# Performance work log

Measured on AMD Instinct MI355X. Metric: run time of the kernel, lower is better.

## Reference

```python
import jax, jax.numpy as jnp
import numpy as np

N_NODES = 50000
N_EDGES = 800000
IN_CH = 128
HEADS = 4
OUT_CH = 32


def setup_inputs() -> dict:
    key = jax.random.key(0)
    k1, k2, k3, k4 = jax.random.split(key, 4)
    x = jax.random.normal(k1, (N_NODES, IN_CH), dtype=jnp.float32)
    edge_index = jax.random.randint(k2, (2, N_EDGES), 0, N_NODES, dtype=jnp.int64)
    # nn.Linear weight [out, in] with xavier-uniform init
    limW = float(np.sqrt(6.0 / (IN_CH + HEADS * OUT_CH)))
    W = jax.random.uniform(k3, (HEADS * OUT_CH, IN_CH), minval=-limW, maxval=limW, dtype=jnp.float32)
    lima = float(np.sqrt(6.0 / (HEADS + 2 * OUT_CH)))
    att = jax.random.uniform(k4, (HEADS, 2 * OUT_CH), minval=-lima, maxval=lima, dtype=jnp.float32)
    bias = jnp.zeros((HEADS * OUT_CH,), dtype=jnp.float32)
    return {"x": x, "edge_index": edge_index, "W": W, "att": att, "bias": bias}


def reference(x, edge_index, W, att, bias):
    n = x.shape[0]
    heads, two_c = att.shape
    out_ch = two_c // 2
    loop = jnp.arange(n, dtype=edge_index.dtype)
    src = jnp.concatenate([edge_index[0], loop])  # [E+n]
    dst = jnp.concatenate([edge_index[1], loop])  # [E+n]
    h = (x @ W.T).reshape(n, heads, out_ch)       # [n, H, C]
    h_src = h[src]                                # [E+n, H, C]
    h_dst = h[dst]                                # [E+n, H, C]
    # e = sum over channels of att applied to [h_src || h_dst]
    e = (jnp.einsum('ehc,hc->eh', h_src, att[:, :out_ch])
         + jnp.einsum('ehc,hc->eh', h_dst, att[:, out_ch:]))  # [E+n, H]
    e = jax.nn.leaky_relu(e, negative_slope=0.2)
    # segment softmax over incoming edges per dst node
    e_max = jax.ops.segment_max(e, dst, num_segments=n)        # [n, H]
    alpha = jnp.exp(e - e_max[dst])                            # [E+n, H]
    a_sum = jax.ops.segment_sum(alpha, dst, num_segments=n)    # [n, H]
    alpha = alpha / jnp.maximum(a_sum[dst], 1e-10)
    weighted = h_src * alpha[..., None]                        # [E+n, H, C]
    out = jax.ops.segment_sum(weighted, dst, num_segments=n)   # [n, H, C]
    out = out.reshape(n, heads * out_ch)                       # concat=True
    return out + bias
```

## Files before the change

kernel.cpp:

```cpp
#include <hip/hip_runtime.h>
#include <hip/hip_bf16.h>
#include <math.h>

#define N_NODES 50000
#define N_EDGES 800000
#define IN_CH   128
#define HEADS   4
#define OUT_CH  32
#define HC      128
#define WROWS   136

#define CB_SHIFT 7
#define CB_NODES 128
#define N_CB     391
#define NBK      128
#define EPB      (N_EDGES / NBK)
#define PCAP     44
#define ND_CAP   48
#define CB_CAP   2560

#define NG_TOT   782
#define NG_A     586
#define NG_B     (NG_TOT - NG_A)

typedef __attribute__((ext_vector_type(8))) short short8;
typedef __attribute__((ext_vector_type(4))) float floatx4;

__device__ __forceinline__ short f2bf(float f) {
    __hip_bfloat16 h = __float2bfloat16(f);
    return *reinterpret_cast<short*>(&h);
}

__global__ __launch_bounds__(256) void kP_prep(
    const float* __restrict__ W, const float* __restrict__ att,
    unsigned short* __restrict__ Wb) {

    const int tid = threadIdx.x;

    {
        int row  = tid >> 1;
        int half = tid & 1;
        const float4* Wr = (const float4*)(W + row * IN_CH + half * 64);
        unsigned short* dp = Wb + row * WROWS + half * 64;
#pragma unroll
        for (int i = 0; i < 16; ++i) {
            float4 v = Wr[i];
            ushort4 p;
            p.x = (unsigned short)f2bf(v.x);
            p.y = (unsigned short)f2bf(v.y);
            p.z = (unsigned short)f2bf(v.z);
            p.w = (unsigned short)f2bf(v.w);
            *(ushort4*)(dp + i * 4) = p;
        }
    }

#pragma unroll
    for (int k = 0; k < 4; ++k) {
        int idx  = tid + k * 256;
        int j    = idx >> 7;
        int i    = idx & 127;
        int head = j & 3;
        int aoff = (j & 4) ? 32 : 0;
        float s = 0.f;
#pragma unroll
        for (int c = 0; c < 32; ++c)
            s = fmaf(W[(head * 32 + c) * IN_CH + i], att[head * 64 + aoff + c], s);
        Wb[(128 + j) * WROWS + i] = (unsigned short)f2bf(s);
    }

    for (int z = tid; z < 8 * WROWS; z += 256) Wb[136 * WROWS + z] = 0;
}

__device__ __forceinline__ void gemm_role(
    short* __restrict__ Wlds, int node_base,
    const float* __restrict__ x, const unsigned short* __restrict__ Wb,
    __hip_bfloat16* __restrict__ hbuf,
    float* __restrict__ asrc, float* __restrict__ adst) {

    const int tid  = threadIdx.x;
    const int wave = tid >> 6;
    const int lane = tid & 63;
    const int col  = lane & 15;
    const int q    = lane >> 4;

#pragma unroll
    for (int i = 0; i < 10; ++i) {
        int off = ((i << 2) + wave) * 64 + lane;
        ((float4*)Wlds)[off] = ((const float4*)Wb)[off];
    }
    __syncthreads();

    const int node0 = node_base + wave * 16;
    const int m  = node0 + col;
    const int mc = min(m, N_NODES - 1);

    floatx4 acc[9];
#pragma unroll
    for (int t = 0; t < 9; ++t) acc[t] = (floatx4){0.f, 0.f, 0.f, 0.f};

#pragma unroll
    for (int ks = 0; ks < 4; ++ks) {
        const float4* xp = (const float4*)(x + (size_t)mc * IN_CH + ks * 32 + q * 8);
        float4 v0 = xp[0];
        float4 v1 = xp[1];
        short8 af;
        af[0] = f2bf(v0.x); af[1] = f2bf(v0.y); af[2] = f2bf(v0.z); af[3] = f2bf(v0.w);
        af[4] = f2bf(v1.x); af[5] = f2bf(v1.y); af[6] = f2bf(v1.z); af[7] = f2bf(v1.w);
#pragma unroll
        for (int t = 0; t < 9; ++t) {
            const short8 bf = *(const short8*)(Wlds + (t * 16 + col) * WROWS + ks * 32 + q * 8);
            acc[t] = __builtin_amdgcn_mfma_f32_16x16x32_bf16(af, bf, acc[t], 0, 0, 0);
        }
    }

#pragma unroll
    for (int r = 0; r < 4; ++r) {
        const int node = node0 + q * 4 + r;
        if (node >= N_NODES) continue;
#pragma unroll
        for (int t = 0; t < 8; ++t)
            hbuf[(size_t)node * HC + t * 16 + col] = __float2bfloat16(acc[t][r]);
        float v8 = acc[8][r];
        if (col < 4)      asrc[node * HEADS + col] = v8;
        else if (col < 8) adst[node * HEADS + col - 4] = v8;
    }
}

__global__ __launch_bounds__(256) void kA_fused(
    const int* __restrict__ src, const int* __restrict__ dst,
    unsigned* __restrict__ priv, int* __restrict__ cnt2,
    const float* __restrict__ x, const unsigned short* __restrict__ Wb,
    __hip_bfloat16* __restrict__ hbuf,
    float* __restrict__ asrc, float* __restrict__ adst) {

    __shared__ float4 smem4[2560];
    const int tid = threadIdx.x;

    if (blockIdx.x < NBK) {
        int* lcnt = (int*)smem4;
        const int blk = blockIdx.x;
        for (int i = tid; i < N_CB; i += 256) lcnt[i] = 0;
        __syncthreads();

        const int e0 = blk * EPB;
        for (int e = e0 + tid; e < e0 + EPB; e += 256) {
            int s = src[e];
            int d = dst[e];
            int cb = d >> CB_SHIFT;
            int pos = atomicAdd(&lcnt[cb], 1);
            if (pos < PCAP)
                priv[((size_t)cb * NBK + blk) * PCAP + pos] =
                    ((unsigned)(d & (CB_NODES - 1)) << 16) | (unsigned)s;
        }
        __syncthreads();
        for (int i = tid; i < N_CB; i += 256)
            cnt2[blk * N_CB + i] = min(lcnt[i], PCAP);
        return;
    }

    gemm_role((short*)smem4, (blockIdx.x - NBK) * 64, x, Wb, hbuf, asrc, adst);
}

__global__ __launch_bounds__(256) void kB_fused(
    const int* __restrict__ cnt2, const unsigned* __restrict__ priv,
    unsigned short* __restrict__ csr16, unsigned* __restrict__ meta,
    const float* __restrict__ x, const unsigned short* __restrict__ Wb,
    __hip_bfloat16* __restrict__ hbuf,
    float* __restrict__ asrc, float* __restrict__ adst) {

    __shared__ float4 smem4[2560];
    const int tid = threadIdx.x;

    if (blockIdx.x >= N_CB) {
        gemm_role((short*)smem4, (NG_A + (int)blockIdx.x - N_CB) * 64,
                  x, Wb, hbuf, asrc, adst);
        return;
    }

    char* smem = (char*)smem4;
    unsigned short* list = (unsigned short*)smem;
    int* lcnt  = (int*)(smem + 12800);
    int* ccnt  = (int*)(smem + 13312);
    int* lpre  = (int*)(smem + 13824);
    int* lcnt2 = (int*)(smem + 14336);

    const int b = blockIdx.x;
    const int node0 = b << CB_SHIFT;
    const int nInB  = min(CB_NODES, N_NODES - node0);

    if (tid < CB_NODES) lcnt[tid] = 0;
    if (tid < NBK) lcnt2[tid] = cnt2[tid * N_CB + b];
    __syncthreads();

    const unsigned* p = priv + (size_t)b * NBK * PCAP;
    for (int idx = tid; idx < NBK * PCAP; idx += 256) {
        int blk = (idx * 5958) >> 18;
        int j   = idx - blk * PCAP;
        if (j < lcnt2[blk]) {
            unsigned ent = p[idx];
            int dl   = ent >> 16;
            int slot = atomicAdd(&lcnt[dl], 1);
            if (slot < ND_CAP) list[dl * ND_CAP + slot] = (unsigned short)(ent & 0xFFFFu);
        }
    }
    __syncthreads();

    if (tid < CB_NODES) { ccnt[tid] = min(lcnt[tid], ND_CAP); lpre[tid] = ccnt[tid]; }
    __syncthreads();
    for (int d = 1; d < CB_NODES; d <<= 1) {
        int v = (tid >= d && tid < CB_NODES) ? lpre[tid - d] : 0;
        __syncthreads();
        if (tid < CB_NODES) lpre[tid] += v;
        __syncthreads();
    }

    if (tid < nInB) {
        int cnt  = ccnt[tid];
        int excl = lpre[tid] - cnt;
        meta[node0 + tid] = (unsigned)(b * CB_CAP + excl) | ((unsigned)cnt << 24);
    }

    const int total = lpre[CB_NODES - 1];
    __syncthreads();
    for (int idx = tid; idx < total; idx += 256) {
        int n = 0;
#pragma unroll
        for (int s = 64; s; s >>= 1)
            if (idx >= lpre[n + s - 1]) n += s;
        int j = idx - (lpre[n] - ccnt[n]);
        csr16[b * CB_CAP + idx] = list[n * ND_CAP + j];
    }
}

__device__ __forceinline__ float edge_w(float t) {
    t = fmaxf(t, 0.2f * t);
    return __expf(t);
}

__global__ __launch_bounds__(256) void kb6_agg(
    const unsigned* __restrict__ meta, const unsigned short* __restrict__ csr16,
    const unsigned* __restrict__ hb, const float* __restrict__ asrc,
    const float* __restrict__ adst, const float* __restrict__ bias,
    float* __restrict__ out) {

    const int node = __builtin_amdgcn_readfirstlane(blockIdx.x * 4 + (threadIdx.x >> 6));
    if (node >= N_NODES) return;
    const int lane = threadIdx.x & 63;
    const int h    = lane >> 4;

    const unsigned mt = meta[node];
    const int cnt = (int)(mt >> 24);
    const unsigned short* p = csr16 + (mt & 0xFFFFFFu);

    const float ad = adst[node * HEADS + h];

    unsigned us = hb[node * 64 + lane];
    float wS = edge_w(asrc[node * HEADS + h] + ad);
    float ds = wS;
    float ax = wS * __uint_as_float(us << 16);
    float ay = wS * __uint_as_float(us & 0xffff0000u);

    int e = 0;
    for (; e + 7 < cnt; e += 8) {
        int s0 = p[e],     s1 = p[e + 1], s2 = p[e + 2], s3 = p[e + 3];
        int s4 = p[e + 4], s5 = p[e + 5], s6 = p[e + 6], s7 = p[e + 7];
        unsigned u0 = hb[s0 * 64 + lane];
        unsigned u1 = hb[s1 * 64 + lane];
        unsigned u2 = hb[s2 * 64 + lane];
        unsigned u3 = hb[s3 * 64 + lane];
        unsigned u4 = hb[s4 * 64 + lane];
        unsigned u5 = hb[s5 * 64 + lane];
        unsigned u6 = hb[s6 * 64 + lane];
        unsigned u7 = hb[s7 * 64 + lane];
        float w0 = edge_w(asrc[s0 * HEADS + h] + ad);
        float w1 = edge_w(asrc[s1 * HEADS + h] + ad);
        float w2 = edge_w(asrc[s2 * HEADS + h] + ad);
        float w3 = edge_w(asrc[s3 * HEADS + h] + ad);
        float w4 = edge_w(asrc[s4 * HEADS + h] + ad);
        float w5 = edge_w(asrc[s5 * HEADS + h] + ad);
        float w6 = edge_w(asrc[s6 * HEADS + h] + ad);
        float w7 = edge_w(asrc[s7 * HEADS + h] + ad);
        ds += ((w0 + w1) + (w2 + w3)) + ((w4 + w5) + (w6 + w7));
        ax = fmaf(w0, __uint_as_float(u0 << 16), ax);
        ay = fmaf(w0, __uint_as_float(u0 & 0xffff0000u), ay);
        ax = fmaf(w1, __uint_as_float(u1 << 16), ax);
        ay = fmaf(w1, __uint_as_float(u1 & 0xffff0000u), ay);
        ax = fmaf(w2, __uint_as_float(u2 << 16), ax);
        ay = fmaf(w2, __uint_as_float(u2 & 0xffff0000u), ay);
        ax = fmaf(w3, __uint_as_float(u3 << 16), ax);
        ay = fmaf(w3, __uint_as_float(u3 & 0xffff0000u), ay);
        ax = fmaf(w4, __uint_as_float(u4 << 16), ax);
        ay = fmaf(w4, __uint_as_float(u4 & 0xffff0000u), ay);
        ax = fmaf(w5, __uint_as_float(u5 << 16), ax);
        ay = fmaf(w5, __uint_as_float(u5 & 0xffff0000u), ay);
        ax = fmaf(w6, __uint_as_float(u6 << 16), ax);
        ay = fmaf(w6, __uint_as_float(u6 & 0xffff0000u), ay);
        ax = fmaf(w7, __uint_as_float(u7 << 16), ax);
        ay = fmaf(w7, __uint_as_float(u7 & 0xffff0000u), ay);
    }
    for (; e + 3 < cnt; e += 4) {
        int s0 = p[e], s1 = p[e + 1], s2 = p[e + 2], s3 = p[e + 3];
        unsigned u0 = hb[s0 * 64 + lane];
        unsigned u1 = hb[s1 * 64 + lane];
        unsigned u2 = hb[s2 * 64 + lane];
        unsigned u3 = hb[s3 * 64 + lane];
        float w0 = edge_w(asrc[s0 * HEADS + h] + ad);
        float w1 = edge_w(asrc[s1 * HEADS + h] + ad);
        float w2 = edge_w(asrc[s2 * HEADS + h] + ad);
        float w3 = edge_w(asrc[s3 * HEADS + h] + ad);
        ds += (w0 + w1) + (w2 + w3);
        ax = fmaf(w0, __uint_as_float(u0 << 16), ax);
        ay = fmaf(w0, __uint_as_float(u0 & 0xffff0000u), ay);
        ax = fmaf(w1, __uint_as_float(u1 << 16), ax);
        ay = fmaf(w1, __uint_as_float(u1 & 0xffff0000u), ay);
        ax = fmaf(w2, __uint_as_float(u2 << 16), ax);
        ay = fmaf(w2, __uint_as_float(u2 & 0xffff0000u), ay);
        ax = fmaf(w3, __uint_as_float(u3 << 16), ax);
        ay = fmaf(w3, __uint_as_float(u3 & 0xffff0000u), ay);
    }
    for (; e < cnt; ++e) {
        int s0 = p[e];
        unsigned u0 = hb[s0 * 64 + lane];
        float w0 = edge_w(asrc[s0 * HEADS + h] + ad);
        ds += w0;
        ax = fmaf(w0, __uint_as_float(u0 << 16), ax);
        ay = fmaf(w0, __uint_as_float(u0 & 0xffff0000u), ay);
    }

    float inv = 1.0f / fmaxf(ds, 1e-10f);
    float2 b = *(const float2*)(bias + lane * 2);
    float2 o;
    o.x = ax * inv + b.x;
    o.y = ay * inv + b.y;
    *(float2*)(out + (size_t)node * HC + lane * 2) = o;
}

extern "C" void kernel_launch(void* const* d_in, const int* in_sizes, int n_in,
                              void* d_out, int out_size, void* d_ws, size_t ws_size,
                              hipStream_t stream) {
    const float* x    = (const float*)d_in[0];
    const int*   ei   = (const int*)d_in[1];
    const float* W    = (const float*)d_in[2];
    const float* att  = (const float*)d_in[3];
    const float* bias = (const float*)d_in[4];
    float* out = (float*)d_out;

    const int* src = ei;
    const int* dst = ei + N_EDGES;

    char* ws = (char*)d_ws;
    __hip_bfloat16* hbuf = (__hip_bfloat16*)ws;
    float*    asrc = (float*)(ws + 12800000);
    float*    adst = (float*)(ws + 13600000);
    unsigned* priv = (unsigned*)(ws + 14400000);
    int*      cnt2 = (int*)(ws + 23208448);
    unsigned short* Wb = (unsigned short*)(ws + 23408640);
    unsigned* meta = (unsigned*)(ws + 23449600);
    unsigned short* csr16 = (unsigned short*)(ws + 23649600);

    kP_prep<<<1, 256, 0, stream>>>(W, att, Wb);
    kA_fused<<<NBK + NG_A, 256, 0, stream>>>(src, dst, priv, cnt2,
                                             x, Wb, hbuf, asrc, adst);
    kB_fused<<<N_CB + NG_B, 256, 0, stream>>>(cnt2, priv, csr16, meta,
                                              x, Wb, hbuf, asrc, adst);
    kb6_agg<<<(N_NODES + 3) / 4, 256, 0, stream>>>(meta, csr16, (const unsigned*)hbuf,
                                                   asrc, adst, bias, out);
}
```

Baseline: 160.3 us.

## Fold weight prep into GEMM blocks, pad CSR lists, vectorize index loads

Drops the single-block prep kernel: every GEMM block now converts W to bf16 and computes the attention-projected rows directly into LDS. This removes one launch and its serialization, at the cost of redundant work in each block. Per-node CSR lists are padded to multiples of 8 so the aggregation kernel can read eight 16-bit source indices with one uint4 load, and the 4-wide remainder loop is removed. The hidden-feature layout is changed to packed pairs of channels 16 apart, and x loads are hoisted ahead of the MFMA loop.

Measured after the change: 163.3 us. No clear change (+1.9%).

```diff
diff --git a/kernel.cpp b/kernel.cpp
--- a/kernel.cpp
+++ b/kernel.cpp
@@ -17,7 +17,7 @@
 #define EPB      (N_EDGES / NBK)
 #define PCAP     44
 #define ND_CAP   48
-#define CB_CAP   2560
+#define CB_CAP   3072
 
 #define NG_TOT   782
 #define NG_A     586
@@ -26,34 +26,37 @@
 typedef __attribute__((ext_vector_type(8))) short short8;
 typedef __attribute__((ext_vector_type(4))) float floatx4;
 
-__device__ __forceinline__ short f2bf(float f) {
+__device__ __forceinline__ unsigned short f2bf(float f) {
     __hip_bfloat16 h = __float2bfloat16(f);
-    return *reinterpret_cast<short*>(&h);
-}
-
-__global__ __launch_bounds__(256) void kP_prep(
-    const float* __restrict__ W, const float* __restrict__ att,
-    unsigned short* __restrict__ Wb) {
-
-    const int tid = threadIdx.x;
+    return *reinterpret_cast<unsigned short*>(&h);
+}
+
+__device__ __forceinline__ void gemm_role(
+    short* __restrict__ Wlds, int node_base,
+    const float* __restrict__ x, const float* __restrict__ W,
+    const float* __restrict__ att,
+    unsigned* __restrict__ hbuf_u,
+    float* __restrict__ asrc, float* __restrict__ adst) {
+
+    const int tid  = threadIdx.x;
+    const int wave = tid >> 6;
+    const int lane = tid & 63;
+    const int col  = lane & 15;
+    const int q    = lane >> 4;
 
     {
         int row  = tid >> 1;
         int half = tid & 1;
         const float4* Wr = (const float4*)(W + row * IN_CH + half * 64);
-        unsigned short* dp = Wb + row * WROWS + half * 64;
+        unsigned short* dp = (unsigned short*)Wlds + row * WROWS + half * 64;
 #pragma unroll
         for (int i = 0; i < 16; ++i) {
             float4 v = Wr[i];
             ushort4 p;
-            p.x = (unsigned short)f2bf(v.x);
-            p.y = (unsigned short)f2bf(v.y);
-            p.z = (unsigned short)f2bf(v.z);
-            p.w = (unsigned short)f2bf(v.w);
+            p.x = f2bf(v.x); p.y = f2bf(v.y); p.z = f2bf(v.z); p.w = f2bf(v.w);
             *(ushort4*)(dp + i * 4) = p;
         }
     }
-
 #pragma unroll
     for (int k = 0; k < 4; ++k) {
         int idx  = tid + k * 256;
@@ -65,44 +68,32 @@
 #pragma unroll
         for (int c = 0; c < 32; ++c)
             s = fmaf(W[(head * 32 + c) * IN_CH + i], att[head * 64 + aoff + c], s);
-        Wb[(128 + j) * WROWS + i] = (unsigned short)f2bf(s);
-    }
-
-    for (int z = tid; z < 8 * WROWS; z += 256) Wb[136 * WROWS + z] = 0;
-}
-
-__device__ __forceinline__ void gemm_role(
-    short* __restrict__ Wlds, int node_base,
-    const float* __restrict__ x, const unsigned short* __restrict__ Wb,
-    __hip_bfloat16* __restrict__ hbuf,
-    float* __restrict__ asrc, float* __restrict__ adst) {
-
-    const int tid  = threadIdx.x;
-    const int wave = tid >> 6;
-    const int lane = tid & 63;
-    const int col  = lane & 15;
-    const int q    = lane >> 4;
-
-#pragma unroll
-    for (int i = 0; i < 10; ++i) {
-        int off = ((i << 2) + wave) * 64 + lane;
-        ((float4*)Wlds)[off] = ((const float4*)Wb)[off];
-    }
+        ((unsigned short*)Wlds)[(128 + j) * WROWS + i] = f2bf(s);
+    }
+    for (int z = tid; z < 8 * WROWS; z += 256)
+        ((unsigned short*)Wlds)[136 * WROWS + z] = 0;
     __syncthreads();
 
     const int node0 = node_base + wave * 16;
     const int m  = node0 + col;
     const int mc = min(m, N_NODES - 1);
 
+    const float4* xb = (const float4*)(x + (size_t)mc * IN_CH);
+    float4 xv[8];
+#pragma unroll
+    for (int ks = 0; ks < 4; ++ks) {
+        xv[2 * ks]     = xb[ks * 8 + q * 2];
+        xv[2 * ks + 1] = xb[ks * 8 + q * 2 + 1];
+    }
+
     floatx4 acc[9];
 #pragma unroll
     for (int t = 0; t < 9; ++t) acc[t] = (floatx4){0.f, 0.f, 0.f, 0.f};
 
 #pragma unroll
     for (int ks = 0; ks < 4; ++ks) {
-        const float4* xp = (const float4*)(x + (size_t)mc * IN_CH + ks * 32 + q * 8);
-        float4 v0 = xp[0];
-        float4 v1 = xp[1];
+        float4 v0 = xv[2 * ks];
+        float4 v1 = xv[2 * ks + 1];
         short8 af;
         af[0] = f2bf(v0.x); af[1] = f2bf(v0.y); af[2] = f2bf(v0.z); af[3] = f2bf(v0.w);
         af[4] = f2bf(v1.x); af[5] = f2bf(v1.y); af[6] = f2bf(v1.z); af[7] = f2bf(v1.w);
@@ -118,8 +109,11 @@
         const int node = node0 + q * 4 + r;
         if (node >= N_NODES) continue;
 #pragma unroll
-        for (int t = 0; t < 8; ++t)
-            hbuf[(size_t)node * HC + t * 16 + col] = __float2bfloat16(acc[t][r]);
+        for (int k = 0; k < 4; ++k) {
+            unsigned pk = (unsigned)f2bf(acc[2 * k][r]) |
+                          ((unsigned)f2bf(acc[2 * k + 1][r]) << 16);
+            hbuf_u[(size_t)node * 64 + k * 16 + col] = pk;
+        }
         float v8 = acc[8][r];
         if (col < 4)      asrc[node * HEADS + col] = v8;
         else if (col < 8) adst[node * HEADS + col - 4] = v8;
@@ -129,15 +123,15 @@
 __global__ __launch_bounds__(256) void kA_fused(
     const int* __restrict__ src, const int* __restrict__ dst,
     unsigned* __restrict__ priv, int* __restrict__ cnt2,
-    const float* __restrict__ x, const unsigned short* __restrict__ Wb,
-    __hip_bfloat16* __restrict__ hbuf,
+    const float* __restrict__ x, const float* __restrict__ W,
+    const float* __restrict__ att, unsigned* __restrict__ hbuf_u,
     float* __restrict__ asrc, float* __restrict__ adst) {
 
-    __shared__ float4 smem4[2560];
+    __shared__ short smem[144 * WROWS];
     const int tid = threadIdx.x;
 
     if (blockIdx.x < NBK) {
-        int* lcnt = (int*)smem4;
+        int* lcnt = (int*)smem;
         const int blk = blockIdx.x;
         for (int i = tid; i < N_CB; i += 256) lcnt[i] = 0;
         __syncthreads();
@@ -158,31 +152,32 @@
         return;
     }
 
-    gemm_role((short*)smem4, (blockIdx.x - NBK) * 64, x, Wb, hbuf, asrc, adst);
+    gemm_role(smem, (blockIdx.x - NBK) * 64, x, W, att, hbuf_u, asrc, adst);
 }
 
 __global__ __launch_bounds__(256) void kB_fused(
     const int* __restrict__ cnt2, const unsigned* __restrict__ priv,
     unsigned short* __restrict__ csr16, unsigned* __restrict__ meta,
-    const float* __restrict__ x, const unsigned short* __restrict__ Wb,
-    __hip_bfloat16* __restrict__ hbuf,
+    const float* __restrict__ x, const float* __restrict__ W,
+    const float* __restrict__ att, unsigned* __restrict__ hbuf_u,
     float* __restrict__ asrc, float* __restrict__ adst) {
 
-    __shared__ float4 smem4[2560];
+    __shared__ short smem[144 * WROWS];
     const int tid = threadIdx.x;
 
     if (blockIdx.x >= N_CB) {
-        gemm_role((short*)smem4, (NG_A + (int)blockIdx.x - N_CB) * 64,
-                  x, Wb, hbuf, asrc, adst);
+        gemm_role(smem, (NG_A + (int)blockIdx.x - N_CB) * 64,
+                  x, W, att, hbuf_u, asrc, adst);
         return;
     }
 
-    char* smem = (char*)smem4;
-    unsigned short* list = (unsigned short*)smem;
-    int* lcnt  = (int*)(smem + 12800);
-    int* ccnt  = (int*)(smem + 13312);
-    int* lpre  = (int*)(smem + 13824);
-    int* lcnt2 = (int*)(smem + 14336);
+    char* sm = (char*)smem;
+    unsigned short* list = (unsigned short*)sm;
+    int* lcnt  = (int*)(sm + 12800);
+    int* ccnt  = (int*)(sm + 13312);
+    int* rcnt  = (int*)(sm + 13824);
+    int* rpre  = (int*)(sm + 14336);
+    int* lcnt2 = (int*)(sm + 14848);
 
     const int b = blockIdx.x;
     const int node0 = b << CB_SHIFT;
@@ -205,30 +200,37 @@
     }
     __syncthreads();
 
-    if (tid < CB_NODES) { ccnt[tid] = min(lcnt[tid], ND_CAP); lpre[tid] = ccnt[tid]; }
+    if (tid < CB_NODES) {
+        int c = min(lcnt[tid], ND_CAP);
+        ccnt[tid] = c;
+        int rc = (c + 7) & ~7;
+        rcnt[tid] = rc;
+        rpre[tid] = rc;
+    }
     __syncthreads();
     for (int d = 1; d < CB_NODES; d <<= 1) {
-        int v = (tid >= d && tid < CB_NODES) ? lpre[tid - d] : 0;
+        int v = (tid >= d && tid < CB_NODES) ? rpre[tid - d] : 0;
         __syncthreads();
-        if (tid < CB_NODES) lpre[tid] += v;
+        if (tid < CB_NODES) rpre[tid] += v;
         __syncthreads();
     }
 
     if (tid < nInB) {
-        int cnt  = ccnt[tid];
-        int excl = lpre[tid] - cnt;
-        meta[node0 + tid] = (unsigned)(b * CB_CAP + excl) | ((unsigned)cnt << 24);
-    }
-
-    const int total = lpre[CB_NODES - 1];
-    __syncthreads();
-    for (int idx = tid; idx < total; idx += 256) {
+        int cnt    = ccnt[tid];
+        int excl_r = rpre[tid] - rcnt[tid];
+        meta[node0 + tid] = (unsigned)(b * CB_CAP + excl_r) | ((unsigned)cnt << 24);
+    }
+
+    const int totalR = rpre[CB_NODES - 1];
+    __syncthreads();
+    for (int idx = tid; idx < totalR; idx += 256) {
         int n = 0;
 #pragma unroll
         for (int s = 64; s; s >>= 1)
-            if (idx >= lpre[n + s - 1]) n += s;
-        int j = idx - (lpre[n] - ccnt[n]);
-        csr16[b * CB_CAP + idx] = list[n * ND_CAP + j];
+            if (idx >= rpre[n + s - 1]) n += s;
+        int j = idx - (rpre[n] - rcnt[n]);
+        if (j < ccnt[n])
+            csr16[b * CB_CAP + idx] = list[n * ND_CAP + j];
     }
 }
 
@@ -247,6 +249,8 @@
     if (node >= N_NODES) return;
     const int lane = threadIdx.x & 63;
     const int h    = lane >> 4;
+    const int c0   = 32 * h + (lane & 15);
+    const int c1   = c0 + 16;
 
     const unsigned mt = meta[node];
     const int cnt = (int)(mt >> 24);
@@ -262,8 +266,11 @@
 
     int e = 0;
     for (; e + 7 < cnt; e += 8) {
-        int s0 = p[e],     s1 = p[e + 1], s2 = p[e + 2], s3 = p[e + 3];
-        int s4 = p[e + 4], s5 = p[e + 5], s6 = p[e + 6], s7 = p[e + 7];
+        uint4 idv = *(const uint4*)(p + e);
+        int s0 = idv.x & 0xFFFF, s1 = idv.x >> 16;
+        int s2 = idv.y & 0xFFFF, s3 = idv.y >> 16;
+        int s4 = idv.z & 0xFFFF, s5 = idv.z >> 16;
+        int s6 = idv.w & 0xFFFF, s7 = idv.w >> 16;
         unsigned u0 = hb[s0 * 64 + lane];
         unsigned u1 = hb[s1 * 64 + lane];
         unsigned u2 = hb[s2 * 64 + lane];
@@ -298,26 +305,6 @@
         ax = fmaf(w7, __uint_as_float(u7 << 16), ax);
         ay = fmaf(w7, __uint_as_float(u7 & 0xffff0000u), ay);
     }
-    for (; e + 3 < cnt; e += 4) {
-        int s0 = p[e], s1 = p[e + 1], s2 = p[e + 2], s3 = p[e + 3];
-        unsigned u0 = hb[s0 * 64 + lane];
-        unsigned u1 = hb[s1 * 64 + lane];
-        unsigned u2 = hb[s2 * 64 + lane];
-        unsigned u3 = hb[s3 * 64 + lane];
-        float w0 = edge_w(asrc[s0 * HEADS + h] + ad);
-        float w1 = edge_w(asrc[s1 * HEADS + h] + ad);
-        float w2 = edge_w(asrc[s2 * HEADS + h] + ad);
-        float w3 = edge_w(asrc[s3 * HEADS + h] + ad);
-        ds += (w0 + w1) + (w2 + w3);
-        ax = fmaf(w0, __uint_as_float(u0 << 16), ax);
-        ay = fmaf(w0, __uint_as_float(u0 & 0xffff0000u), ay);
-        ax = fmaf(w1, __uint_as_float(u1 << 16), ax);
-        ay = fmaf(w1, __uint_as_float(u1 & 0xffff0000u), ay);
-        ax = fmaf(w2, __uint_as_float(u2 << 16), ax);
-        ay = fmaf(w2, __uint_as_float(u2 & 0xffff0000u), ay);
-        ax = fmaf(w3, __uint_as_float(u3 << 16), ax);
-        ay = fmaf(w3, __uint_as_float(u3 & 0xffff0000u), ay);
-    }
     for (; e < cnt; ++e) {
         int s0 = p[e];
         unsigned u0 = hb[s0 * 64 + lane];
@@ -328,11 +315,8 @@
     }
 
     float inv = 1.0f / fmaxf(ds, 1e-10f);
-    float2 b = *(const float2*)(bias + lane * 2);
-    float2 o;
-    o.x = ax * inv + b.x;
-    o.y = ay * inv + b.y;
-    *(float2*)(out + (size_t)node * HC + lane * 2) = o;
+    out[(size_t)node * HC + c0] = ax * inv + bias[c0];
+    out[(size_t)node * HC + c1] = ay * inv + bias[c1];
 }
 
 extern "C" void kernel_launch(void* const* d_in, const int* in_sizes, int n_in,
@@ -349,20 +333,18 @@
     const int* dst = ei + N_EDGES;
 
     char* ws = (char*)d_ws;
-    __hip_bfloat16* hbuf = (__hip_bfloat16*)ws;
+    unsigned* hbuf_u = (unsigned*)ws;
     float*    asrc = (float*)(ws + 12800000);
     float*    adst = (float*)(ws + 13600000);
     unsigned* priv = (unsigned*)(ws + 14400000);
     int*      cnt2 = (int*)(ws + 23208448);
-    unsigned short* Wb = (unsigned short*)(ws + 23408640);
-    unsigned* meta = (unsigned*)(ws + 23449600);
-    unsigned short* csr16 = (unsigned short*)(ws + 23649600);
-
-    kP_prep<<<1, 256, 0, stream>>>(W, att, Wb);
+    unsigned* meta = (unsigned*)(ws + 23408640);
+    unsigned short* csr16 = (unsigned short*)(ws + 23608640);
+
     kA_fused<<<NBK + NG_A, 256, 0, stream>>>(src, dst, priv, cnt2,
-                                             x, Wb, hbuf, asrc, adst);
+                                             x, W, att, hbuf_u, asrc, adst);
     kB_fused<<<N_CB + NG_B, 256, 0, stream>>>(cnt2, priv, csr16, meta,
-                                              x, Wb, hbuf, asrc, adst);
-    kb6_agg<<<(N_NODES + 3) / 4, 256, 0, stream>>>(meta, csr16, (const unsigned*)hbuf,
+                                              x, W, att, hbuf_u, asrc, adst);
+    kb6_agg<<<(N_NODES + 3) / 4, 256, 0, stream>>>(meta, csr16, hbuf_u,
                                                    asrc, adst, bias, out);
 }
```
